# Kernel optimization log

Measured on AMD Instinct MI355X. Metric: run time of the kernel, lower is better.

Reference implementation:

```python
import jax, jax.numpy as jnp
import numpy as np

B, T, I, H, A, V, OOV = 256, 1, 256, 512, 400, 50000, 50


def _xavier(k, shape):
    fan_out, fan_in = shape[0], shape[-1]
    std = (2.0 / (fan_in + fan_out)) ** 0.5
    return jax.random.normal(k, shape, jnp.float32) * std


def setup_inputs() -> dict:
    key = jax.random.key(0)
    ks = jax.random.split(key, 24)
    return {
        "x": jax.random.normal(ks[0], (B, T, I), jnp.float32),
        "y": jax.random.randint(ks[1], (B, T), 0, V),  # teacher-forcing arg, unused in forward
        "encoder_outputs": jax.random.normal(ks[2], (B, A, A), jnp.float32),
        "encoder_cell": jax.random.normal(ks[3], (B, H), jnp.float32),  # encoder_in[1], unused
        "encoder_state": jax.random.normal(ks[4], (B, H), jnp.float32),
        "max_oov_nums": OOV,
        "ids": jax.random.randint(ks[5], (B, A), 0, V + OOV),
        # LSTM params (PyTorch layout: gates ordered i, f, g, o)
        "W_ih": jax.random.normal(ks[6], (4 * H, I), jnp.float32) * (1.0 / np.sqrt(H)),
        "W_hh": jax.random.normal(ks[7], (4 * H, H), jnp.float32) * (1.0 / np.sqrt(H)),
        "b_ih": jnp.zeros((4 * H,), jnp.float32),
        "b_hh": jnp.zeros((4 * H,), jnp.float32),
        # attention
        "Wh_w": _xavier(ks[8], (A, H)), "Wh_b": jnp.zeros((A,), jnp.float32),
        "Ws_w": _xavier(ks[9], (A, H)), "Ws_b": jnp.zeros((A,), jnp.float32),
        "v": jax.random.normal(ks[10], (A,), jnp.float32),
        # vocab head
        "fc1_w": _xavier(ks[11], (2 * H, H + A)), "fc1_b": jnp.zeros((2 * H,), jnp.float32),
        "fc2_w": _xavier(ks[12], (V, 2 * H)), "fc2_b": jnp.zeros((V,), jnp.float32),
        # p_gen gates (no bias)
        "pg1_w": _xavier(ks[13], (1, I)),
        "pg2_w": _xavier(ks[14], (1, A)),
        "pg3_w": _xavier(ks[15], (1, H)),
    }


def reference(x, y, encoder_outputs, encoder_cell, encoder_state, max_oov_nums, ids,
              W_ih, W_hh, b_ih, b_hh, Wh_w, Wh_b, Ws_w, Ws_b, v,
              fc1_w, fc1_b, fc2_w, fc2_b, pg1_w, pg2_w, pg3_w):
    x0 = x[:, 0, :]  # [B, I] single decode step
    # --- single LSTM step with zero initial (h, c) ---
    gates = x0 @ W_ih.T + b_ih + b_hh  # h0 = 0 so W_hh term vanishes
    i_g, f_g, g_g, o_g = jnp.split(gates, 4, axis=-1)
    c = jax.nn.sigmoid(i_g) * jnp.tanh(g_g)  # c0 = 0
    h = jax.nn.sigmoid(o_g) * jnp.tanh(c)    # decoder_state [B, H]
    # --- Bahdanau-style attention (first step: coverage is zeros, w_c has no bias) ---
    e = jnp.tanh(encoder_state @ Wh_w.T + Wh_b + h @ Ws_w.T + Ws_b)  # [B, A]
    attention = v * jax.nn.softmax(e, axis=-1)  # [B, A]
    # --- context vector: weighted sum over encoder outputs ---
    context = jnp.einsum('ba,bae->be', attention, encoder_outputs)  # [B, A]
    # --- vocab distribution ---
    dec_in = jnp.concatenate([context, h], axis=-1)  # [B, A+H]
    p_vocab = jax.nn.softmax((dec_in @ fc1_w.T + fc1_b) @ fc2_w.T + fc2_b, axis=-1)  # [B, V]
    # --- generation probability gate ---
    gen = jax.nn.sigmoid(context @ pg2_w[0] + x0 @ pg1_w[0] + h @ pg3_w[0])  # [B]
    p_vocab = gen[:, None] * p_vocab
    att_copy = (1.0 - gen)[:, None] * attention
    # --- extended vocab + copy scatter-add ---
    p = jnp.concatenate([p_vocab, jnp.zeros((p_vocab.shape[0], max_oov_nums), p_vocab.dtype)], axis=-1)
    rows = jnp.arange(p.shape[0])[:, None]
    p = p.at[rows, ids].add(att_copy)
    return p
```

## Files before the change

kernel.cpp:

```cpp
#include <hip/hip_runtime.h>
#include <hip/hip_bf16.h>
#include <math.h>

#define BB      256
#define I_DIM   256
#define H_DIM   512
#define A_DIM   400
#define V_DIM   50000
#define OOV     50
#define VP      50050
#define FC1_IN  912
#define FC1_OUT 1024
#define FC2_K   1024

typedef unsigned short u16;
typedef unsigned int   u32;
typedef __attribute__((ext_vector_type(8))) short  short8;
typedef __attribute__((ext_vector_type(4))) float  float4_;

__device__ __forceinline__ u16 f2bf(float f) {
    u32 u = __builtin_bit_cast(u32, f);
    u32 r = (u + 0x7FFFu + ((u >> 16) & 1u)) >> 16;
    return (u16)r;
}

__global__ __launch_bounds__(256)
void sgemm32(const float* __restrict__ Am, const float* __restrict__ Wm,
             float* __restrict__ Cm, const float* __restrict__ bias0,
             const float* __restrict__ bias1, int M, int N, int K,
             int accumulate, int act)
{
    __shared__ float As[16][33];
    __shared__ float Bs[16][33];
    int t  = threadIdx.x;
    int tx = t & 15, ty = t >> 4;
    int m0 = blockIdx.y * 32, n0 = blockIdx.x * 32;
    int lm = t >> 3;
    int lk = (t & 7) * 2;
    const float* aptr = Am + (size_t)(m0 + lm) * K + lk;
    const float* wptr = Wm + (size_t)(n0 + lm) * K + lk;
    bool wvalid = (n0 + lm) < N;
    float c00 = 0.f, c01 = 0.f, c10 = 0.f, c11 = 0.f;

    for (int k0 = 0; k0 < K; k0 += 16) {
        float a0 = aptr[0], a1 = aptr[1];
        float w0 = wvalid ? wptr[0] : 0.f;
        float w1 = wvalid ? wptr[1] : 0.f;
        __syncthreads();
        As[lk][lm] = a0;  As[lk + 1][lm] = a1;
        Bs[lk][lm] = w0;  Bs[lk + 1][lm] = w1;
        __syncthreads();
#pragma unroll
        for (int k = 0; k < 16; ++k) {
            float av0 = As[k][ty], av1 = As[k][ty + 16];
            float bv0 = Bs[k][tx], bv1 = Bs[k][tx + 16];
            c00 += av0 * bv0;  c01 += av0 * bv1;
            c10 += av1 * bv0;  c11 += av1 * bv1;
        }
        aptr += 16; wptr += 16;
    }

    int r0 = m0 + ty, r1 = m0 + ty + 16;
    int cc0 = n0 + tx, cc1 = n0 + tx + 16;
    float accv[2][2] = {{c00, c01}, {c10, c11}};
    int rows[2] = {r0, r1};
    int cols[2] = {cc0, cc1};
#pragma unroll
    for (int i = 0; i < 2; ++i)
#pragma unroll
        for (int j = 0; j < 2; ++j) {
            int c = cols[j];
            if (c < N) {
                size_t idx = (size_t)rows[i] * N + c;
                float v = accv[i][j];
                if (accumulate) v += Cm[idx];
                if (bias0) v += bias0[c];
                if (bias1) v += bias1[c];
                if (act == 1) v = tanhf(v);
                Cm[idx] = v;
            }
        }
}

__global__ __launch_bounds__(256)
void lstm_h_kernel(const float* __restrict__ G, float* __restrict__ hbuf,
                   float* __restrict__ dec_in)
{
    int idx = blockIdx.x * 256 + threadIdx.x;
    int b = idx >> 9, j = idx & 511;
    const float* g = G + (size_t)b * 2048;
    float ig = g[j], gg = g[1024 + j], og = g[1536 + j];
    float si = 1.f / (1.f + expf(-ig));
    float so = 1.f / (1.f + expf(-og));
    float c  = si * tanhf(gg);
    float h  = so * tanhf(c);
    hbuf[idx] = h;
    dec_in[(size_t)b * FC1_IN + A_DIM + j] = h;
}

__global__ __launch_bounds__(256)
void att_kernel(const float* __restrict__ e, const float* __restrict__ vvec,
                float* __restrict__ att)
{
    __shared__ float s_ex[A_DIM];
    __shared__ float red[256];
    int b = blockIdx.x, t = threadIdx.x;
    const float* er = e + (size_t)b * A_DIM;
    float local = 0.f;
    for (int a = t; a < A_DIM; a += 256) {
        float ex = expf(er[a]);
        s_ex[a] = ex; local += ex;
    }
    red[t] = local; __syncthreads();
    for (int s = 128; s > 0; s >>= 1) {
        if (t < s) red[t] += red[t + s];
        __syncthreads();
    }
    float inv = 1.f / red[0];
    for (int a = t; a < A_DIM; a += 256)
        att[(size_t)b * A_DIM + a] = vvec[a] * s_ex[a] * inv;
}

__global__ __launch_bounds__(512)
void ctx_gen_kernel(const float* __restrict__ att, const float* __restrict__ enc,
                    const float* __restrict__ x, const float* __restrict__ h,
                    const float* __restrict__ pg1, const float* __restrict__ pg2,
                    const float* __restrict__ pg3,
                    float* __restrict__ dec_in, float* __restrict__ gen)
{
    __shared__ float s_att[A_DIM];
    __shared__ float red[512];
    int b = blockIdx.x, t = threadIdx.x;
    for (int a = t; a < A_DIM; a += 512) s_att[a] = att[(size_t)b * A_DIM + a];
    __syncthreads();
    float acc = 0.f;
    if (t < A_DIM) {
        const float* ep = enc + (size_t)b * (A_DIM * A_DIM) + t;
#pragma unroll 4
        for (int a = 0; a < A_DIM; ++a) acc += s_att[a] * ep[(size_t)a * A_DIM];
        dec_in[(size_t)b * FC1_IN + t] = acc;
    }
    float local = 0.f;
    if (t < A_DIM) local += acc * pg2[t];
    if (t < I_DIM) local += x[(size_t)b * I_DIM + t] * pg1[t];
    local += h[(size_t)b * H_DIM + t] * pg3[t];
    red[t] = local; __syncthreads();
    for (int s = 256; s > 0; s >>= 1) {
        if (t < s) red[t] += red[t + s];
        __syncthreads();
    }
    if (t == 0) gen[b] = 1.f / (1.f + expf(-red[0]));
}

__global__ __launch_bounds__(256)
void cvt_kernel(const float* __restrict__ hid, u16* __restrict__ hb)
{
    int idx = blockIdx.x * 256 + threadIdx.x;
    hb[idx] = f2bf(hid[idx]);
}

__global__ __launch_bounds__(256)
void fc2_kernel(const u16* __restrict__ hb, const float* __restrict__ W,
                const float* __restrict__ bias, float* __restrict__ out,
                float* __restrict__ sums)
{
    __shared__ __align__(16) u16 Ws[64][72];
    int t = threadIdx.x;
    int wv = t >> 6, lane = t & 63;
    int lm = lane & 15, lk = lane >> 4;
    int n0 = blockIdx.x * 64;
    int row_base = wv * 64;

    float4_ acc[4][4];
#pragma unroll
    for (int mi = 0; mi < 4; ++mi)
#pragma unroll
        for (int ni = 0; ni < 4; ++ni)
            acc[mi][ni] = (float4_){0.f, 0.f, 0.f, 0.f};

    int sn  = t >> 2;
    int skq = (t & 3) * 16;
    bool svalid = (n0 + sn) < V_DIM;
    const float* wsrc = W + (size_t)(n0 + sn) * FC2_K + skq;

    for (int kt = 0; kt < FC2_K / 64; ++kt) {
        float4_ wreg[4];
        if (svalid) {
            const float4_* p = (const float4_*)(wsrc + kt * 64);
            wreg[0] = p[0]; wreg[1] = p[1]; wreg[2] = p[2]; wreg[3] = p[3];
        } else {
#pragma unroll
            for (int i = 0; i < 4; ++i) wreg[i] = (float4_){0.f, 0.f, 0.f, 0.f};
        }
        __syncthreads();
        short8 wlo, whi;
#pragma unroll
        for (int i = 0; i < 4; ++i) {
            wlo[i]     = (short)f2bf(wreg[0][i]);
            wlo[4 + i] = (short)f2bf(wreg[1][i]);
            whi[i]     = (short)f2bf(wreg[2][i]);
            whi[4 + i] = (short)f2bf(wreg[3][i]);
        }
        *(short8*)&Ws[sn][skq]     = wlo;
        *(short8*)&Ws[sn][skq + 8] = whi;
        __syncthreads();

#pragma unroll
        for (int ks = 0; ks < 2; ++ks) {
            short8 af[4], bfr[4];
#pragma unroll
            for (int mi = 0; mi < 4; ++mi)
                af[mi] = *(const short8*)(hb + (size_t)(row_base + mi * 16 + lm) * FC2_K
                                          + kt * 64 + ks * 32 + lk * 8);
#pragma unroll
            for (int ni = 0; ni < 4; ++ni)
                bfr[ni] = *(const short8*)&Ws[ni * 16 + lm][ks * 32 + lk * 8];
#pragma unroll
            for (int mi = 0; mi < 4; ++mi)
#pragma unroll
                for (int ni = 0; ni < 4; ++ni)
                    acc[mi][ni] = __builtin_amdgcn_mfma_f32_16x16x32_bf16(
                        af[mi], bfr[ni], acc[mi][ni], 0, 0, 0);
        }
    }

#pragma unroll
    for (int mi = 0; mi < 4; ++mi) {
        int r_base = row_base + mi * 16 + lk * 4;
        float s[4] = {0.f, 0.f, 0.f, 0.f};
#pragma unroll
        for (int ni = 0; ni < 4; ++ni) {
            int col = n0 + ni * 16 + lm;
            if (col < V_DIM) {
                float bcol = bias[col];
                float4_ a = acc[mi][ni];
#pragma unroll
                for (int r = 0; r < 4; ++r) {
                    float ev = expf(a[r] + bcol);
                    out[(size_t)(r_base + r) * VP + col] = ev;
                    s[r] += ev;
                }
            }
        }
#pragma unroll
        for (int off = 1; off < 16; off <<= 1) {
#pragma unroll
            for (int r = 0; r < 4; ++r) s[r] += __shfl_xor(s[r], off);
        }
        if (lm == 0) {
#pragma unroll
            for (int r = 0; r < 4; ++r) atomicAdd(&sums[r_base + r], s[r]);
        }
    }
}

__global__ __launch_bounds__(256)
void rescale_kernel(float* __restrict__ out, const float* __restrict__ gen,
                    const float* __restrict__ sums)
{
    int idx = (blockIdx.x * 256 + threadIdx.x) * 2;
    int b = idx / VP;
    int c = idx - b * VP;
    float2 v = *(float2*)(out + idx);
    float scale = gen[b] / sums[b];
    v.x = (c     < V_DIM) ? v.x * scale : 0.f;
    v.y = (c + 1 < V_DIM) ? v.y * scale : 0.f;
    *(float2*)(out + idx) = v;
}

__global__ __launch_bounds__(256)
void scatter_kernel(const int* __restrict__ ids, const float* __restrict__ att,
                    const float* __restrict__ gen, float* __restrict__ out)
{
    int idx = blockIdx.x * 256 + threadIdx.x;
    int b = idx / A_DIM;
    float val = (1.f - gen[b]) * att[idx];
    atomicAdd(out + (size_t)b * VP + ids[idx], val);
}

extern "C" void kernel_launch(void* const* d_in, const int* in_sizes, int n_in,
                              void* d_out, int out_size, void* d_ws, size_t ws_size,
                              hipStream_t stream)
{
    const float* x         = (const float*)d_in[0];
    const float* enc       = (const float*)d_in[2];
    const float* enc_state = (const float*)d_in[4];
    const int*   ids       = (const int*)  d_in[6];
    const float* W_ih      = (const float*)d_in[7];
    const float* b_ih      = (const float*)d_in[9];
    const float* b_hh      = (const float*)d_in[10];
    const float* Wh_w      = (const float*)d_in[11];
    const float* Wh_b      = (const float*)d_in[12];
    const float* Ws_w      = (const float*)d_in[13];
    const float* Ws_b      = (const float*)d_in[14];
    const float* vvec      = (const float*)d_in[15];
    const float* fc1_w     = (const float*)d_in[16];
    const float* fc1_b     = (const float*)d_in[17];
    const float* fc2_w     = (const float*)d_in[18];
    const float* fc2_b     = (const float*)d_in[19];
    const float* pg1       = (const float*)d_in[20];
    const float* pg2       = (const float*)d_in[21];
    const float* pg3       = (const float*)d_in[22];
    float* out = (float*)d_out;

    float* ws    = (float*)d_ws;
    float* gates = ws;
    float* hbuf  = gates + 256 * 2048;
    float* ebuf  = hbuf  + 256 * 512;
    float* attb  = ebuf  + 256 * 400;
    float* dec   = attb  + 256 * 400;
    float* hid   = dec   + 256 * 912;
    float* genb  = hid   + 256 * 1024;
    float* sums  = genb  + 256;
    u16*   hbf   = (u16*)(sums + 256);

    sgemm32<<<dim3(64, 8), 256, 0, stream>>>(x, W_ih, gates, b_ih, b_hh,
                                             BB, 2048, I_DIM, 0, 0);
    lstm_h_kernel<<<512, 256, 0, stream>>>(gates, hbuf, dec);
    sgemm32<<<dim3(13, 8), 256, 0, stream>>>(enc_state, Wh_w, ebuf, Wh_b, nullptr,
                                             BB, A_DIM, H_DIM, 0, 0);
    sgemm32<<<dim3(13, 8), 256, 0, stream>>>(hbuf, Ws_w, ebuf, Ws_b, nullptr,
                                             BB, A_DIM, H_DIM, 1, 1);
    att_kernel<<<BB, 256, 0, stream>>>(ebuf, vvec, attb);
    ctx_gen_kernel<<<BB, 512, 0, stream>>>(attb, enc, x, hbuf, pg1, pg2, pg3,
                                           dec, genb);
    sgemm32<<<dim3(32, 8), 256, 0, stream>>>(dec, fc1_w, hid, fc1_b, nullptr,
                                             BB, FC1_OUT, FC1_IN, 0, 0);
    cvt_kernel<<<1024, 256, 0, stream>>>(hid, hbf);
    hipMemsetAsync(sums, 0, BB * sizeof(float), stream);
    fc2_kernel<<<782, 256, 0, stream>>>(hbf, fc2_w, fc2_b, out, sums);
    rescale_kernel<<<(BB * VP) / 512, 256, 0, stream>>>(out, genb, sums);
    scatter_kernel<<<(BB * A_DIM) / 256, 256, 0, stream>>>(ids, attb, genb, out);
}
```

Measured before the change: 758.4 us.

## Double-buffer fc2 weight tiles and widen block to 512 threads

```diff
diff --git a/kernel.cpp b/kernel.cpp
--- a/kernel.cpp
+++ b/kernel.cpp
@@ -159,73 +159,88 @@
     hb[idx] = f2bf(hid[idx]);
 }
 
-__global__ __launch_bounds__(256)
+__global__ __launch_bounds__(512)
 void fc2_kernel(const u16* __restrict__ hb, const float* __restrict__ W,
                 const float* __restrict__ bias, float* __restrict__ out,
                 float* __restrict__ sums)
 {
-    __shared__ __align__(16) u16 Ws[64][72];
+    __shared__ __align__(16) u16 Ws[2][64][72];
     int t = threadIdx.x;
     int wv = t >> 6, lane = t & 63;
     int lm = lane & 15, lk = lane >> 4;
     int n0 = blockIdx.x * 64;
-    int row_base = wv * 64;
-
-    float4_ acc[4][4];
-#pragma unroll
-    for (int mi = 0; mi < 4; ++mi)
+    int row_base = wv * 32;
+
+    float4_ acc[2][4];
+#pragma unroll
+    for (int mi = 0; mi < 2; ++mi)
 #pragma unroll
         for (int ni = 0; ni < 4; ++ni)
             acc[mi][ni] = (float4_){0.f, 0.f, 0.f, 0.f};
 
-    int sn  = t >> 2;
-    int skq = (t & 3) * 16;
+    int sn = t >> 3;
+    int sk = (t & 7) * 8;
     bool svalid = (n0 + sn) < V_DIM;
-    const float* wsrc = W + (size_t)(n0 + sn) * FC2_K + skq;
+    const float* wsrc = W + (size_t)(n0 + sn) * FC2_K + sk;
+
+    {
+        float4_ w0 = (float4_){0.f,0.f,0.f,0.f}, w1 = w0;
+        if (svalid) {
+            const float4_* p = (const float4_*)wsrc;
+            w0 = p[0]; w1 = p[1];
+        }
+        short8 wb;
+#pragma unroll
+        for (int i = 0; i < 4; ++i) {
+            wb[i]     = (short)f2bf(w0[i]);
+            wb[4 + i] = (short)f2bf(w1[i]);
+        }
+        *(short8*)&Ws[0][sn][sk] = wb;
+    }
+    __syncthreads();
 
     for (int kt = 0; kt < FC2_K / 64; ++kt) {
-        float4_ wreg[4];
-        if (svalid) {
-            const float4_* p = (const float4_*)(wsrc + kt * 64);
-            wreg[0] = p[0]; wreg[1] = p[1]; wreg[2] = p[2]; wreg[3] = p[3];
-        } else {
-#pragma unroll
-            for (int i = 0; i < 4; ++i) wreg[i] = (float4_){0.f, 0.f, 0.f, 0.f};
-        }
-        __syncthreads();
-        short8 wlo, whi;
-#pragma unroll
-        for (int i = 0; i < 4; ++i) {
-            wlo[i]     = (short)f2bf(wreg[0][i]);
-            wlo[4 + i] = (short)f2bf(wreg[1][i]);
-            whi[i]     = (short)f2bf(wreg[2][i]);
-            whi[4 + i] = (short)f2bf(wreg[3][i]);
-        }
-        *(short8*)&Ws[sn][skq]     = wlo;
-        *(short8*)&Ws[sn][skq + 8] = whi;
-        __syncthreads();
-
+        int cur = kt & 1;
+        float4_ w0 = (float4_){0.f,0.f,0.f,0.f}, w1 = w0;
+        bool pf = (kt < FC2_K / 64 - 1);
+        if (pf && svalid) {
+            const float4_* p = (const float4_*)(wsrc + (kt + 1) * 64);
+            w0 = p[0]; w1 = p[1];
+        }
+        short8 af[2][2];
+#pragma unroll
+        for (int mi = 0; mi < 2; ++mi)
+#pragma unroll
+            for (int ks = 0; ks < 2; ++ks)
+                af[mi][ks] = *(const short8*)(hb + (size_t)(row_base + mi * 16 + lm) * FC2_K
+                                              + kt * 64 + ks * 32 + lk * 8);
 #pragma unroll
         for (int ks = 0; ks < 2; ++ks) {
-            short8 af[4], bfr[4];
-#pragma unroll
-            for (int mi = 0; mi < 4; ++mi)
-                af[mi] = *(const short8*)(hb + (size_t)(row_base + mi * 16 + lm) * FC2_K
-                                          + kt * 64 + ks * 32 + lk * 8);
+            short8 bfr[4];
 #pragma unroll
             for (int ni = 0; ni < 4; ++ni)
-                bfr[ni] = *(const short8*)&Ws[ni * 16 + lm][ks * 32 + lk * 8];
-#pragma unroll
-            for (int mi = 0; mi < 4; ++mi)
+                bfr[ni] = *(const short8*)&Ws[cur][ni * 16 + lm][ks * 32 + lk * 8];
+#pragma unroll
+            for (int mi = 0; mi < 2; ++mi)
 #pragma unroll
                 for (int ni = 0; ni < 4; ++ni)
                     acc[mi][ni] = __builtin_amdgcn_mfma_f32_16x16x32_bf16(
-                        af[mi], bfr[ni], acc[mi][ni], 0, 0, 0);
-        }
-    }
-
-#pragma unroll
-    for (int mi = 0; mi < 4; ++mi) {
+                        af[mi][ks], bfr[ni], acc[mi][ni], 0, 0, 0);
+        }
+        if (pf) {
+            short8 wb;
+#pragma unroll
+            for (int i = 0; i < 4; ++i) {
+                wb[i]     = (short)f2bf(w0[i]);
+                wb[4 + i] = (short)f2bf(w1[i]);
+            }
+            *(short8*)&Ws[cur ^ 1][sn][sk] = wb;
+        }
+        __syncthreads();
+    }
+
+#pragma unroll
+    for (int mi = 0; mi < 2; ++mi) {
         int r_base = row_base + mi * 16 + lk * 4;
         float s[4] = {0.f, 0.f, 0.f, 0.f};
 #pragma unroll
@@ -328,7 +343,7 @@
                                              BB, FC1_OUT, FC1_IN, 0, 0);
     cvt_kernel<<<1024, 256, 0, stream>>>(hid, hbf);
     hipMemsetAsync(sums, 0, BB * sizeof(float), stream);
-    fc2_kernel<<<782, 256, 0, stream>>>(hbf, fc2_w, fc2_b, out, sums);
+    fc2_kernel<<<782, 512, 0, stream>>>(hbf, fc2_w, fc2_b, out, sums);
     rescale_kernel<<<(BB * VP) / 512, 256, 0, stream>>>(out, genb, sums);
     scatter_kernel<<<(BB * A_DIM) / 256, 256, 0, stream>>>(ids, attb, genb, out);
 }
```

New measurement: 710.6 us. 6.3% less time.
